# Performance work log

Hardware: AMD Instinct MI355X
Metric: run time of the kernel (lower is better)

The kernel has to match this reference:

```python
import jax, jax.numpy as jnp
import numpy as np
import math

V, D, NL, P, B, L = 32000, 512, 4, 8, 2, 2048

def _ln(x, g, b, eps=1e-5):
    m = x.mean(-1, keepdims=True)
    v = ((x - m) ** 2).mean(-1, keepdims=True)
    return (x - m) / jnp.sqrt(v + eps) * g + b

def setup_inputs() -> dict:
    key = jax.random.key(0)
    ks = jax.random.split(key, 20)
    r = lambda k, shp, s: jax.random.normal(k, shp, dtype=jnp.float32) * s
    return {
        "tokens": jax.random.randint(ks[0], (B, L), 0, V),
        "embed": r(ks[1], (V, D), 0.02),
        "ln_scale": jnp.ones((NL, D), jnp.float32),
        "ln_bias": jnp.zeros((NL, D), jnp.float32),
        "phase_W": r(ks[2], (NL, D, P), 1.0 / math.sqrt(D)),
        "phase_b": jnp.zeros((NL, P), jnp.float32),
        "amp_W": r(ks[3], (NL, D, P), 1.0 / math.sqrt(D)),
        "amp_b": jnp.zeros((NL, P), jnp.float32),
        "value_W": r(ks[4], (NL, D, D), 1.0 / math.sqrt(D)),
        "value_b": jnp.zeros((NL, D), jnp.float32),
        "out_ln_scale": jnp.ones((NL, D), jnp.float32),
        "out_ln_bias": jnp.zeros((NL, D), jnp.float32),
        "out_W": r(ks[5], (NL, D, D), 1.0 / math.sqrt(D)),
        "out_b": jnp.zeros((NL, D), jnp.float32),
        "normout_scale": jnp.ones((D,), jnp.float32),
        "normout_bias": jnp.zeros((D,), jnp.float32),
        "head_W": r(ks[6], (D, V), 1.0 / math.sqrt(D)),
        "head_b": jnp.zeros((V,), jnp.float32),
    }

def _phasor(x, pW, pb, aW, ab, vW, vb, oLNs, oLNb, oW, ob):
    # x: [B,L,D]
    phase = jnp.tanh(x @ pW + pb) * jnp.pi            # [B,L,P]
    amp = jax.nn.softplus(x @ aW + ab) + 0.1          # [B,L,P]
    value = x @ vW + vb                               # [B,L,D]
    # (value[...,None,:] * cos_p[...,:,None] * amp[...,:,None]).sum(-2)
    # == value * sum_p(amp * cos_p)  -- identical math, no [B,L,P,D] intermediate
    coef_r = (amp * jnp.cos(phase)).sum(-1, keepdims=True)
    coef_i = (amp * jnp.sin(phase)).sum(-1, keepdims=True)
    mem_r = jnp.cumsum(value * coef_r, axis=1)
    mem_i = jnp.cumsum(value * coef_i, axis=1)
    retrieved = (mem_r + mem_i) / math.sqrt(x.shape[1])
    return x + (_ln(retrieved, oLNs, oLNb) @ oW + ob)

def reference(tokens, embed, ln_scale, ln_bias, phase_W, phase_b, amp_W, amp_b,
              value_W, value_b, out_ln_scale, out_ln_bias, out_W, out_b,
              normout_scale, normout_bias, head_W, head_b):
    h = embed[tokens]                                 # [B,L,D]
    for i in range(NL):
        hn = _ln(h, ln_scale[i], ln_bias[i])
        h = h + _phasor(hn, phase_W[i], phase_b[i], amp_W[i], amp_b[i],
                        value_W[i], value_b[i], out_ln_scale[i], out_ln_bias[i],
                        out_W[i], out_b[i])
    return _ln(h, normout_scale, normout_bias) @ head_W + head_b  # [B,L,V]
```

## Files before the change

### kernel.cpp

```cpp
#include <hip/hip_runtime.h>
#include <math.h>

#define D 512
#define P 8
#define NL 4
#define BB 2
#define LL 2048
#define VV 32000
#define MTOK (BB*LL)
#define CH 128
#define NCH (LL/CH)

__device__ __forceinline__ float softplusf(float x){
    if (x > 20.f) return x;
    return log1pf(expf(x));
}

__device__ __forceinline__ unsigned short f2bf(float f){
    unsigned int u = __float_as_uint(f);
    unsigned int r = (u + 0x7fffu + ((u >> 16) & 1u)) >> 16;
    return (unsigned short)r;
}
__device__ __forceinline__ float bf2f(unsigned short h){
    return __uint_as_float((unsigned int)h << 16);
}

typedef __attribute__((ext_vector_type(8))) short short8;
typedef __attribute__((ext_vector_type(4))) float f32x4;

__device__ __forceinline__ void gload16(const void* g, void* l){
    __builtin_amdgcn_global_load_lds(
        (const __attribute__((address_space(1))) void*)g,
        (__attribute__((address_space(3))) void*)l, 16, 0, 0);
}

__global__ void gather_kernel(const int* __restrict__ tokens,
                              const float* __restrict__ embed,
                              float* __restrict__ h){
    int t = blockIdx.x;
    int tok = tokens[t];
    const float4* src = (const float4*)(embed + (size_t)tok * D);
    float4* dst = (float4*)(h + (size_t)t * D);
    dst[threadIdx.x] = src[threadIdx.x];
}

__global__ void ln_kernel(const float* __restrict__ x,
                          const float* __restrict__ g,
                          const float* __restrict__ b,
                          float* __restrict__ y){
    int t = blockIdx.x;
    int tid = threadIdx.x;
    const float4* xr = (const float4*)(x + (size_t)t * D);
    float4 v = xr[tid];
    float s = v.x + v.y + v.z + v.w;
    float q = v.x*v.x + v.y*v.y + v.z*v.z + v.w*v.w;
    #pragma unroll
    for (int off = 32; off; off >>= 1){
        s += __shfl_down(s, off);
        q += __shfl_down(q, off);
    }
    __shared__ float red[4];
    int wid = tid >> 6, lane = tid & 63;
    if (lane == 0){ red[wid] = s; red[2 + wid] = q; }
    __syncthreads();
    float mean = (red[0] + red[1]) * (1.f / D);
    float var  = (red[2] + red[3]) * (1.f / D) - mean * mean;
    float rstd = rsqrtf(var + 1e-5f);
    float4 gg = ((const float4*)g)[tid];
    float4 bb = ((const float4*)b)[tid];
    float4 o;
    o.x = (v.x - mean) * rstd * gg.x + bb.x;
    o.y = (v.y - mean) * rstd * gg.y + bb.y;
    o.z = (v.z - mean) * rstd * gg.z + bb.z;
    o.w = (v.w - mean) * rstd * gg.w + bb.w;
    ((float4*)(y + (size_t)t * D))[tid] = o;
}

__global__ void proj_kernel(const float* __restrict__ hn,
                            const float* __restrict__ pW, const float* __restrict__ pb,
                            const float* __restrict__ aW, const float* __restrict__ ab,
                            float* __restrict__ cbuf){
    int wid = threadIdx.x >> 6;
    int lane = threadIdx.x & 63;
    int t = blockIdx.x * 4 + wid;
    const float* x = hn + (size_t)t * D;
    float ph[P] = {0.f,0.f,0.f,0.f,0.f,0.f,0.f,0.f};
    float am[P] = {0.f,0.f,0.f,0.f,0.f,0.f,0.f,0.f};
    int d0 = lane * 8;
    #pragma unroll
    for (int j = 0; j < 8; j++){
        float xv = x[d0 + j];
        const float* pr = pW + (size_t)(d0 + j) * P;
        const float* ar = aW + (size_t)(d0 + j) * P;
        #pragma unroll
        for (int p = 0; p < P; p++){ ph[p] += xv * pr[p]; am[p] += xv * ar[p]; }
    }
    #pragma unroll
    for (int off = 32; off; off >>= 1){
        #pragma unroll
        for (int p = 0; p < P; p++){
            ph[p] += __shfl_down(ph[p], off);
            am[p] += __shfl_down(am[p], off);
        }
    }
    if (lane == 0){
        float c = 0.f;
        #pragma unroll
        for (int p = 0; p < P; p++){
            float phase = tanhf(ph[p] + pb[p]) * 3.14159265358979323846f;
            float amp = softplusf(am[p] + ab[p]) + 0.1f;
            c += amp * (cosf(phase) + sinf(phase));
        }
        cbuf[t] = c;
    }
}

__global__ __launch_bounds__(256) void gemm_kernel(
    const float* __restrict__ A, const float* __restrict__ B,
    const float* __restrict__ bias, const float* __restrict__ rowscale,
    const float* __restrict__ R1, const float* __restrict__ R2,
    float* __restrict__ C, int M, int N, int K)
{
    __shared__ float As[16][64];
    __shared__ float Bs[16][64];
    int bn = blockIdx.x * 64, bm = blockIdx.y * 64;
    int tid = threadIdx.x;
    int tx = tid & 15, ty = tid >> 4;
    float acc[4][4] = {};
    int arow = tid >> 2, acol = (tid & 3) * 4;
    int brow = tid >> 4, bcol = (tid & 15) * 4;
    for (int k0 = 0; k0 < K; k0 += 16){
        float4 av = *(const float4*)(A + (size_t)(bm + arow) * K + k0 + acol);
        As[acol + 0][arow] = av.x; As[acol + 1][arow] = av.y;
        As[acol + 2][arow] = av.z; As[acol + 3][arow] = av.w;
        float4 bv = *(const float4*)(B + (size_t)(k0 + brow) * N + bn + bcol);
        *(float4*)(&Bs[brow][bcol]) = bv;
        __syncthreads();
        #pragma unroll
        for (int k = 0; k < 16; k++){
            float ar[4], br[4];
            #pragma unroll
            for (int i = 0; i < 4; i++) ar[i] = As[k][ty * 4 + i];
            #pragma unroll
            for (int j = 0; j < 4; j++) br[j] = Bs[k][tx * 4 + j];
            #pragma unroll
            for (int i = 0; i < 4; i++)
                #pragma unroll
                for (int j = 0; j < 4; j++)
                    acc[i][j] += ar[i] * br[j];
        }
        __syncthreads();
    }
    float4 bi = *(const float4*)(bias + bn + tx * 4);
    #pragma unroll
    for (int i = 0; i < 4; i++){
        int m = bm + ty * 4 + i;
        float rs = rowscale ? rowscale[m] : 1.f;
        size_t idx = (size_t)m * N + bn + tx * 4;
        float4 v;
        v.x = (acc[i][0] + bi.x) * rs;
        v.y = (acc[i][1] + bi.y) * rs;
        v.z = (acc[i][2] + bi.z) * rs;
        v.w = (acc[i][3] + bi.w) * rs;
        if (R1){
            float4 r = *(const float4*)(R1 + idx);
            v.x += r.x; v.y += r.y; v.z += r.z; v.w += r.w;
        }
        if (R2){
            float4 r = *(const float4*)(R2 + idx);
            v.x += r.x; v.y += r.y; v.z += r.z; v.w += r.w;
        }
        *(float4*)(C + idx) = v;
    }
}

__global__ void scan1_kernel(const float* __restrict__ s, float* __restrict__ partial){
    int id = blockIdx.x;
    int b = id >> 5;
    int rem = id & 31;
    int ch = rem >> 1;
    int d = (rem & 1) * 256 + threadIdx.x;
    const float* base = s + ((size_t)b * LL + (size_t)ch * CH) * D + d;
    float sum = 0.f;
    for (int l = 0; l < CH; l++) sum += base[(size_t)l * D];
    partial[((size_t)b * D + d) * NCH + ch] = sum;
}

__global__ void scan2_kernel(float* __restrict__ partial){
    int t = blockIdx.x * 256 + threadIdx.x;
    float run = 0.f;
    float* p = partial + (size_t)t * NCH;
    for (int ch = 0; ch < NCH; ch++){ float v = p[ch]; p[ch] = run; run += v; }
}

__global__ void scan3_kernel(const float* __restrict__ s, const float* __restrict__ partial,
                             float* __restrict__ ret){
    int id = blockIdx.x;
    int b = id >> 5;
    int rem = id & 31;
    int ch = rem >> 1;
    int d = (rem & 1) * 256 + threadIdx.x;
    float run = partial[((size_t)b * D + d) * NCH + ch];
    const float invs = 0.022097086912079608f;
    const float* base = s + ((size_t)b * LL + (size_t)ch * CH) * D + d;
    float* obase = ret + ((size_t)b * LL + (size_t)ch * CH) * D + d;
    for (int l = 0; l < CH; l++){
        run += base[(size_t)l * D];
        obase[(size_t)l * D] = run * invs;
    }
}


__global__ void convA_kernel(const float* __restrict__ x, unsigned short* __restrict__ A2){
    int t = blockIdx.x, tid = threadIdx.x;
    float4 v = ((const float4*)(x + (size_t)t * D))[tid];
    ushort4 h, l;
    h.x = f2bf(v.x); l.x = f2bf(v.x - bf2f(h.x));
    h.y = f2bf(v.y); l.y = f2bf(v.y - bf2f(h.y));
    h.z = f2bf(v.z); l.z = f2bf(v.z - bf2f(h.z));
    h.w = f2bf(v.w); l.w = f2bf(v.w - bf2f(h.w));
    size_t o = (size_t)t * 1024 + (size_t)tid * 4;
    *(ushort4*)(A2 + o)       = h;
    *(ushort4*)(A2 + o + 512) = l;
}

__global__ __launch_bounds__(256) void convB_kernel(const float* __restrict__ Bsrc,
                                                    unsigned short* __restrict__ Bt){
    __shared__ float tile[64][65];
    int n0 = blockIdx.x * 64;
    int k0 = blockIdx.y * 64;
    int tid = threadIdx.x;
    #pragma unroll
    for (int ph = 0; ph < 4; ph++){
        int idx = ph * 256 + tid;
        int r = idx >> 4;
        int c4 = idx & 15;
        float4 v = *(const float4*)(Bsrc + (size_t)(k0 + r) * VV + n0 + c4 * 4);
        tile[r][c4*4+0] = v.x; tile[r][c4*4+1] = v.y;
        tile[r][c4*4+2] = v.z; tile[r][c4*4+3] = v.w;
    }
    __syncthreads();
    int nn = tid >> 2;
    int kb = tid & 3;
    size_t orow = (size_t)(n0 + nn) * 1024;
    #pragma unroll
    for (int j4 = 0; j4 < 4; j4++){
        int kk = kb * 16 + j4 * 4;
        ushort4 h4, l4;
        float v0 = tile[kk + 0][nn], v1 = tile[kk + 1][nn];
        float v2 = tile[kk + 2][nn], v3 = tile[kk + 3][nn];
        h4.x = f2bf(v0); l4.x = f2bf(v0 - bf2f(h4.x));
        h4.y = f2bf(v1); l4.y = f2bf(v1 - bf2f(h4.y));
        h4.z = f2bf(v2); l4.z = f2bf(v2 - bf2f(h4.z));
        h4.w = f2bf(v3); l4.w = f2bf(v3 - bf2f(h4.w));
        size_t o = orow + (size_t)(k0 + kk);
        *(ushort4*)(Bt + o)       = h4;
        *(ushort4*)(Bt + o + 512) = l4;
    }
}

__global__ __launch_bounds__(256) void head_mfma_kernel(
    const unsigned short* __restrict__ A2,
    const unsigned short* __restrict__ Bt,
    const float* __restrict__ bias,
    float* __restrict__ C)
{
    __shared__ unsigned short As[2][4096];
    __shared__ unsigned short Bs[2][4096];
    const int bm = blockIdx.x * 128;
    const int bn = blockIdx.y * 128;
    const int tid  = threadIdx.x;
    const int lane = tid & 63;
    const int wave = tid >> 6;
    const int wr = wave >> 1, wc = wave & 1;

    const int srow = wave * 32 + (lane >> 2);
    const int scol = (lane & 3) * 8;
    const unsigned short* Ag0 = A2 + (size_t)(bm + srow) * 1024 + scol;
    const unsigned short* Ag1 = Ag0 + (size_t)16 * 1024;
    const unsigned short* Bg0 = Bt + (size_t)(bn + srow) * 1024 + scol;
    const unsigned short* Bg1 = Bg0 + (size_t)16 * 1024;

    f32x4 acc[4][4] = {};

    const int frow = lane & 15;
    const int kq   = lane >> 4;
    const int abase = (wr * 64 + frow) * 32 + kq * 8;
    const int bbase = (wc * 64 + frow) * 32 + kq * 8;

    auto stagef = [&](int buf, int ko){
        int ka = (ko < 512) ? ko : ko - 512;
        int kb = (ko >= 1024) ? ko - 1024 : ko;
        gload16(Ag0 + ka, &As[buf][wave * 1024]);
        gload16(Ag1 + ka, &As[buf][wave * 1024 + 512]);
        gload16(Bg0 + kb, &Bs[buf][wave * 1024]);
        gload16(Bg1 + kb, &Bs[buf][wave * 1024 + 512]);
    };

    stagef(0, 0);
    __syncthreads();

    for (int t = 0; t < 48; ++t){
        int cur = t & 1;
        if (t < 47) stagef(cur ^ 1, (t + 1) * 32);
        const unsigned short* Ab = &As[cur][0];
        const unsigned short* Bb = &Bs[cur][0];
        short8 af[4], bv[4];
        #pragma unroll
        for (int f = 0; f < 4; f++){
            af[f] = *(const short8*)(Ab + abase + f * 512);
            bv[f] = *(const short8*)(Bb + bbase + f * 512);
        }
        #pragma unroll
        for (int i = 0; i < 4; i++)
            #pragma unroll
            for (int j = 0; j < 4; j++)
                acc[i][j] = __builtin_amdgcn_mfma_f32_16x16x32_bf16(af[i], bv[j], acc[i][j], 0, 0, 0);
        __syncthreads();
    }

    #pragma unroll
    for (int j = 0; j < 4; j++){
        int col = bn + wc * 64 + j * 16 + frow;
        float bi = bias[col];
        #pragma unroll
        for (int i = 0; i < 4; i++){
            int row0 = bm + wr * 64 + i * 16 + kq * 4;
            #pragma unroll
            for (int r = 0; r < 4; r++)
                C[(size_t)(row0 + r) * VV + col] = acc[i][j][r] + bi;
        }
    }
}

extern "C" void kernel_launch(void* const* d_in, const int* in_sizes, int n_in,
                              void* d_out, int out_size, void* d_ws, size_t ws_size,
                              hipStream_t stream) {
    const int*   tokens        = (const int*)  d_in[0];
    const float* embed         = (const float*)d_in[1];
    const float* ln_scale      = (const float*)d_in[2];
    const float* ln_bias       = (const float*)d_in[3];
    const float* phase_W       = (const float*)d_in[4];
    const float* phase_b       = (const float*)d_in[5];
    const float* amp_W         = (const float*)d_in[6];
    const float* amp_b         = (const float*)d_in[7];
    const float* value_W       = (const float*)d_in[8];
    const float* value_b       = (const float*)d_in[9];
    const float* out_ln_scale  = (const float*)d_in[10];
    const float* out_ln_bias   = (const float*)d_in[11];
    const float* out_W         = (const float*)d_in[12];
    const float* out_b         = (const float*)d_in[13];
    const float* normout_scale = (const float*)d_in[14];
    const float* normout_bias  = (const float*)d_in[15];
    const float* head_W        = (const float*)d_in[16];
    const float* head_b        = (const float*)d_in[17];
    float* out = (float*)d_out;

    float* ws   = (float*)d_ws;
    float* h    = ws;
    float* hn   = h    + (size_t)MTOK*D;
    float* sbuf = hn   + (size_t)MTOK*D;
    float* rbuf = sbuf + (size_t)MTOK*D;
    float* cbuf = rbuf + (size_t)MTOK*D;
    float* part = cbuf + MTOK;

    size_t used_f = (size_t)4*MTOK*D + MTOK + (size_t)BB*D*NCH;
    size_t abf_f  = (used_f + 255) & ~(size_t)255;
    size_t bbf_f  = abf_f + (size_t)MTOK * 1024 / 2;
    size_t need   = (bbf_f + (size_t)VV * 1024 / 2) * sizeof(float);
    unsigned short* Abf = (unsigned short*)(ws + abf_f);
    unsigned short* Bbf = (unsigned short*)(ws + bbf_f);
    bool fast = (ws_size >= need);

    gather_kernel<<<MTOK, 128, 0, stream>>>(tokens, embed, h);

    for (int i = 0; i < NL; i++){
        ln_kernel<<<MTOK, 128, 0, stream>>>(h, ln_scale + i*D, ln_bias + i*D, hn);
        proj_kernel<<<MTOK/4, 256, 0, stream>>>(hn,
            phase_W + (size_t)i*D*P, phase_b + i*P,
            amp_W   + (size_t)i*D*P, amp_b   + i*P, cbuf);
        dim3 g1(D/64, MTOK/64);
        gemm_kernel<<<g1, 256, 0, stream>>>(hn, value_W + (size_t)i*D*D, value_b + i*D,
                                            cbuf, nullptr, nullptr, sbuf, MTOK, D, D);
        scan1_kernel<<<64, 256, 0, stream>>>(sbuf, part);
        scan2_kernel<<<4, 256, 0, stream>>>(part);
        scan3_kernel<<<64, 256, 0, stream>>>(sbuf, part, rbuf);
        ln_kernel<<<MTOK, 128, 0, stream>>>(rbuf, out_ln_scale + i*D, out_ln_bias + i*D, rbuf);
        gemm_kernel<<<g1, 256, 0, stream>>>(rbuf, out_W + (size_t)i*D*D, out_b + i*D,
                                            nullptr, h, hn, h, MTOK, D, D);
    }

    ln_kernel<<<MTOK, 128, 0, stream>>>(h, normout_scale, normout_bias, hn);

    if (fast){
        convA_kernel<<<MTOK, 128, 0, stream>>>(hn, Abf);
        convB_kernel<<<dim3(VV/64, D/64), 256, 0, stream>>>(head_W, Bbf);
        head_mfma_kernel<<<dim3(MTOK/128, VV/128), 256, 0, stream>>>(Abf, Bbf, head_b, out);
    } else {
        dim3 gh(VV/64, MTOK/64);
        gemm_kernel<<<gh, 256, 0, stream>>>(hn, head_W, head_b,
                                            nullptr, nullptr, nullptr, out, MTOK, VV, D);
    }
}
```

Baseline: 1.669 ms.

## Switch matmuls to fp16 split-A MFMA and move layer GEMMs to tensor cores

Replaces the bf16 hi/lo split on both operands with fp16, splitting only the activations into hi+lo while keeping weights as a single fp16 copy. This cuts the head GEMM K loop from 48 to 32 steps and halves the weight buffer. It also adds a gemm16 MFMA kernel plus a convW pre-conversion, so the per-layer value and output GEMMs run on matrix cores instead of the fp32 gemm_kernel. The scan chunk size drops from 128 to 32 for more parallelism. Rounding the weights to fp16 alone reduces accuracy, and the extra convA passes per layer add memory traffic.

```diff
diff --git a/kernel.cpp b/kernel.cpp
--- a/kernel.cpp
+++ b/kernel.cpp
@@ -8,7 +8,7 @@
 #define LL 2048
 #define VV 32000
 #define MTOK (BB*LL)
-#define CH 128
+#define CH 32
 #define NCH (LL/CH)
 
 __device__ __forceinline__ float softplusf(float x){
@@ -16,16 +16,16 @@
     return log1pf(expf(x));
 }
 
-__device__ __forceinline__ unsigned short f2bf(float f){
-    unsigned int u = __float_as_uint(f);
-    unsigned int r = (u + 0x7fffu + ((u >> 16) & 1u)) >> 16;
-    return (unsigned short)r;
-}
-__device__ __forceinline__ float bf2f(unsigned short h){
-    return __uint_as_float((unsigned int)h << 16);
-}
-
-typedef __attribute__((ext_vector_type(8))) short short8;
+__device__ __forceinline__ unsigned short f2h_u(float f){
+    _Float16 h = (_Float16)f;
+    union { _Float16 h; unsigned short u; } cv; cv.h = h; return cv.u;
+}
+__device__ __forceinline__ float h_lo_residual(float f, unsigned short hu){
+    union { unsigned short u; _Float16 h; } cv; cv.u = hu;
+    return f - (float)cv.h;
+}
+
+typedef __attribute__((ext_vector_type(8))) _Float16 f16x8;
 typedef __attribute__((ext_vector_type(4))) float f32x4;
 
 __device__ __forceinline__ void gload16(const void* g, void* l){
@@ -176,8 +176,8 @@
 
 __global__ void scan1_kernel(const float* __restrict__ s, float* __restrict__ partial){
     int id = blockIdx.x;
-    int b = id >> 5;
-    int rem = id & 31;
+    int b = id >> 7;
+    int rem = id & 127;
     int ch = rem >> 1;
     int d = (rem & 1) * 256 + threadIdx.x;
     const float* base = s + ((size_t)b * LL + (size_t)ch * CH) * D + d;
@@ -196,8 +196,8 @@
 __global__ void scan3_kernel(const float* __restrict__ s, const float* __restrict__ partial,
                              float* __restrict__ ret){
     int id = blockIdx.x;
-    int b = id >> 5;
-    int rem = id & 31;
+    int b = id >> 7;
+    int rem = id & 127;
     int ch = rem >> 1;
     int d = (rem & 1) * 256 + threadIdx.x;
     float run = partial[((size_t)b * D + d) * NCH + ch];
@@ -215,10 +215,10 @@
     int t = blockIdx.x, tid = threadIdx.x;
     float4 v = ((const float4*)(x + (size_t)t * D))[tid];
     ushort4 h, l;
-    h.x = f2bf(v.x); l.x = f2bf(v.x - bf2f(h.x));
-    h.y = f2bf(v.y); l.y = f2bf(v.y - bf2f(h.y));
-    h.z = f2bf(v.z); l.z = f2bf(v.z - bf2f(h.z));
-    h.w = f2bf(v.w); l.w = f2bf(v.w - bf2f(h.w));
+    h.x = f2h_u(v.x); l.x = f2h_u(h_lo_residual(v.x, h.x));
+    h.y = f2h_u(v.y); l.y = f2h_u(h_lo_residual(v.y, h.y));
+    h.z = f2h_u(v.z); l.z = f2h_u(h_lo_residual(v.z, h.z));
+    h.w = f2h_u(v.w); l.w = f2h_u(h_lo_residual(v.w, h.w));
     size_t o = (size_t)t * 1024 + (size_t)tid * 4;
     *(ushort4*)(A2 + o)       = h;
     *(ushort4*)(A2 + o + 512) = l;
@@ -242,20 +242,51 @@
     __syncthreads();
     int nn = tid >> 2;
     int kb = tid & 3;
-    size_t orow = (size_t)(n0 + nn) * 1024;
+    size_t orow = (size_t)(n0 + nn) * 512;
     #pragma unroll
     for (int j4 = 0; j4 < 4; j4++){
         int kk = kb * 16 + j4 * 4;
-        ushort4 h4, l4;
-        float v0 = tile[kk + 0][nn], v1 = tile[kk + 1][nn];
-        float v2 = tile[kk + 2][nn], v3 = tile[kk + 3][nn];
-        h4.x = f2bf(v0); l4.x = f2bf(v0 - bf2f(h4.x));
-        h4.y = f2bf(v1); l4.y = f2bf(v1 - bf2f(h4.y));
-        h4.z = f2bf(v2); l4.z = f2bf(v2 - bf2f(h4.z));
-        h4.w = f2bf(v3); l4.w = f2bf(v3 - bf2f(h4.w));
-        size_t o = orow + (size_t)(k0 + kk);
-        *(ushort4*)(Bt + o)       = h4;
-        *(ushort4*)(Bt + o + 512) = l4;
+        ushort4 h4;
+        h4.x = f2h_u(tile[kk + 0][nn]);
+        h4.y = f2h_u(tile[kk + 1][nn]);
+        h4.z = f2h_u(tile[kk + 2][nn]);
+        h4.w = f2h_u(tile[kk + 3][nn]);
+        *(ushort4*)(Bt + orow + (size_t)(k0 + kk)) = h4;
+    }
+}
+
+__global__ __launch_bounds__(256) void convW_kernel(const float* __restrict__ vW,
+                                                    const float* __restrict__ oW,
+                                                    unsigned short* __restrict__ Wt){
+    __shared__ float tile[64][65];
+    int m = blockIdx.z;
+    const float* src = (m < NL) ? (vW + (size_t)m * D * D) : (oW + (size_t)(m - NL) * D * D);
+    unsigned short* dst = Wt + (size_t)m * D * D;
+    int n0 = blockIdx.x * 64;
+    int k0 = blockIdx.y * 64;
+    int tid = threadIdx.x;
+    #pragma unroll
+    for (int ph = 0; ph < 4; ph++){
+        int idx = ph * 256 + tid;
+        int r = idx >> 4;
+        int c4 = idx & 15;
+        float4 v = *(const float4*)(src + (size_t)(k0 + r) * D + n0 + c4 * 4);
+        tile[r][c4*4+0] = v.x; tile[r][c4*4+1] = v.y;
+        tile[r][c4*4+2] = v.z; tile[r][c4*4+3] = v.w;
+    }
+    __syncthreads();
+    int nn = tid >> 2;
+    int kb = tid & 3;
+    size_t orow = (size_t)(n0 + nn) * 512;
+    #pragma unroll
+    for (int j4 = 0; j4 < 4; j4++){
+        int kk = kb * 16 + j4 * 4;
+        ushort4 h4;
+        h4.x = f2h_u(tile[kk + 0][nn]);
+        h4.y = f2h_u(tile[kk + 1][nn]);
+        h4.z = f2h_u(tile[kk + 2][nn]);
+        h4.w = f2h_u(tile[kk + 3][nn]);
+        *(ushort4*)(dst + orow + (size_t)(k0 + kk)) = h4;
     }
 }
 
@@ -278,8 +309,8 @@
     const int scol = (lane & 3) * 8;
     const unsigned short* Ag0 = A2 + (size_t)(bm + srow) * 1024 + scol;
     const unsigned short* Ag1 = Ag0 + (size_t)16 * 1024;
-    const unsigned short* Bg0 = Bt + (size_t)(bn + srow) * 1024 + scol;
-    const unsigned short* Bg1 = Bg0 + (size_t)16 * 1024;
+    const unsigned short* Bg0 = Bt + (size_t)(bn + srow) * 512 + scol;
+    const unsigned short* Bg1 = Bg0 + (size_t)16 * 512;
 
     f32x4 acc[4][4] = {};
 
@@ -289,10 +320,9 @@
     const int bbase = (wc * 64 + frow) * 32 + kq * 8;
 
     auto stagef = [&](int buf, int ko){
-        int ka = (ko < 512) ? ko : ko - 512;
-        int kb = (ko >= 1024) ? ko - 1024 : ko;
-        gload16(Ag0 + ka, &As[buf][wave * 1024]);
-        gload16(Ag1 + ka, &As[buf][wave * 1024 + 512]);
+        int kb = ko & 511;
+        gload16(Ag0 + ko, &As[buf][wave * 1024]);
+        gload16(Ag1 + ko, &As[buf][wave * 1024 + 512]);
         gload16(Bg0 + kb, &Bs[buf][wave * 1024]);
         gload16(Bg1 + kb, &Bs[buf][wave * 1024 + 512]);
     };
@@ -300,22 +330,22 @@
     stagef(0, 0);
     __syncthreads();
 
-    for (int t = 0; t < 48; ++t){
+    for (int t = 0; t < 32; ++t){
         int cur = t & 1;
-        if (t < 47) stagef(cur ^ 1, (t + 1) * 32);
+        if (t < 31) stagef(cur ^ 1, (t + 1) * 32);
         const unsigned short* Ab = &As[cur][0];
         const unsigned short* Bb = &Bs[cur][0];
-        short8 af[4], bv[4];
+        f16x8 af[4], bv[4];
         #pragma unroll
         for (int f = 0; f < 4; f++){
-            af[f] = *(const short8*)(Ab + abase + f * 512);
-            bv[f] = *(const short8*)(Bb + bbase + f * 512);
+            af[f] = *(const f16x8*)(const void*)(Ab + abase + f * 512);
+            bv[f] = *(const f16x8*)(const void*)(Bb + bbase + f * 512);
         }
         #pragma unroll
         for (int i = 0; i < 4; i++)
             #pragma unroll
             for (int j = 0; j < 4; j++)
-                acc[i][j] = __builtin_amdgcn_mfma_f32_16x16x32_bf16(af[i], bv[j], acc[i][j], 0, 0, 0);
+                acc[i][j] = __builtin_amdgcn_mfma_f32_16x16x32_f16(af[i], bv[j], acc[i][j], 0, 0, 0);
         __syncthreads();
     }
 
@@ -329,6 +359,86 @@
             #pragma unroll
             for (int r = 0; r < 4; r++)
                 C[(size_t)(row0 + r) * VV + col] = acc[i][j][r] + bi;
+        }
+    }
+}
+
+__global__ __launch_bounds__(256) void gemm16_kernel(
+    const unsigned short* __restrict__ A2,
+    const unsigned short* __restrict__ Bt,
+    const float* __restrict__ bias,
+    const float* __restrict__ rowscale,
+    const float* __restrict__ R1, const float* __restrict__ R2,
+    float* __restrict__ C)
+{
+    __shared__ unsigned short As[2][4096];
+    __shared__ unsigned short Bs[2][2048];
+    const int bm = blockIdx.x * 128;
+    const int bn = blockIdx.y * 64;
+    const int tid  = threadIdx.x;
+    const int lane = tid & 63;
+    const int wave = tid >> 6;
+    const int wr = wave >> 1, wc = wave & 1;
+
+    const int srow = wave * 32 + (lane >> 2);
+    const int srb  = wave * 16 + (lane >> 2);
+    const int scol = (lane & 3) * 8;
+    const unsigned short* Ag0 = A2 + (size_t)(bm + srow) * 1024 + scol;
+    const unsigned short* Ag1 = Ag0 + (size_t)16 * 1024;
+    const unsigned short* Bg  = Bt + (size_t)(bn + srb) * 512 + scol;
+
+    f32x4 acc[4][2] = {};
+
+    const int frow = lane & 15;
+    const int kq   = lane >> 4;
+    const int abase = (wr * 64 + frow) * 32 + kq * 8;
+    const int bbase = (wc * 32 + frow) * 32 + kq * 8;
+
+    auto stagef = [&](int buf, int ko){
+        int kb = ko & 511;
+        gload16(Ag0 + ko, &As[buf][wave * 1024]);
+        gload16(Ag1 + ko, &As[buf][wave * 1024 + 512]);
+        gload16(Bg + kb,  &Bs[buf][wave * 512]);
+    };
+
+    stagef(0, 0);
+    __syncthreads();
+
+    for (int t = 0; t < 32; ++t){
+        int cur = t & 1;
+        if (t < 31) stagef(cur ^ 1, (t + 1) * 32);
+        const unsigned short* Ab = &As[cur][0];
+        const unsigned short* Bb = &Bs[cur][0];
+        f16x8 af[4], bv[2];
+        #pragma unroll
+        for (int f = 0; f < 4; f++) af[f] = *(const f16x8*)(const void*)(Ab + abase + f * 512);
+        #pragma unroll
+        for (int f = 0; f < 2; f++) bv[f] = *(const f16x8*)(const void*)(Bb + bbase + f * 512);
+        #pragma unroll
+        for (int i = 0; i < 4; i++)
+            #pragma unroll
+            for (int j = 0; j < 2; j++)
+                acc[i][j] = __builtin_amdgcn_mfma_f32_16x16x32_f16(af[i], bv[j], acc[i][j], 0, 0, 0);
+        __syncthreads();
+    }
+
+    #pragma unroll
+    for (int j = 0; j < 2; j++){
+        int col = bn + wc * 32 + j * 16 + frow;
+        float bi = bias[col];
+        #pragma unroll
+        for (int i = 0; i < 4; i++){
+            int row0 = bm + wr * 64 + i * 16 + kq * 4;
+            #pragma unroll
+            for (int r = 0; r < 4; r++){
+                int row = row0 + r;
+                size_t idx = (size_t)row * D + col;
+                float v = acc[i][j][r] + bi;
+                if (rowscale) v *= rowscale[row];
+                if (R1) v += R1[idx];
+                if (R2) v += R2[idx];
+                C[idx] = v;
+            }
         }
     }
 }
@@ -366,35 +476,53 @@
 
     size_t used_f = (size_t)4*MTOK*D + MTOK + (size_t)BB*D*NCH;
     size_t abf_f  = (used_f + 255) & ~(size_t)255;
-    size_t bbf_f  = abf_f + (size_t)MTOK * 1024 / 2;
-    size_t need   = (bbf_f + (size_t)VV * 1024 / 2) * sizeof(float);
+    size_t bbf_f  = abf_f + (size_t)MTOK * 512;
+    size_t wt_f   = bbf_f + (size_t)VV * 256;
+    size_t need   = (wt_f + (size_t)2*NL*D*D/2) * sizeof(float);
     unsigned short* Abf = (unsigned short*)(ws + abf_f);
     unsigned short* Bbf = (unsigned short*)(ws + bbf_f);
+    unsigned short* Wt  = (unsigned short*)(ws + wt_f);
     bool fast = (ws_size >= need);
 
     gather_kernel<<<MTOK, 128, 0, stream>>>(tokens, embed, h);
+    if (fast){
+        convW_kernel<<<dim3(D/64, D/64, 2*NL), 256, 0, stream>>>(value_W, out_W, Wt);
+        convB_kernel<<<dim3(VV/64, D/64), 256, 0, stream>>>(head_W, Bbf);
+    }
 
     for (int i = 0; i < NL; i++){
         ln_kernel<<<MTOK, 128, 0, stream>>>(h, ln_scale + i*D, ln_bias + i*D, hn);
         proj_kernel<<<MTOK/4, 256, 0, stream>>>(hn,
             phase_W + (size_t)i*D*P, phase_b + i*P,
             amp_W   + (size_t)i*D*P, amp_b   + i*P, cbuf);
-        dim3 g1(D/64, MTOK/64);
-        gemm_kernel<<<g1, 256, 0, stream>>>(hn, value_W + (size_t)i*D*D, value_b + i*D,
-                                            cbuf, nullptr, nullptr, sbuf, MTOK, D, D);
-        scan1_kernel<<<64, 256, 0, stream>>>(sbuf, part);
+        if (fast){
+            convA_kernel<<<MTOK, 128, 0, stream>>>(hn, Abf);
+            gemm16_kernel<<<dim3(MTOK/128, D/64), 256, 0, stream>>>(Abf,
+                Wt + (size_t)i*D*D, value_b + i*D, cbuf, nullptr, nullptr, sbuf);
+        } else {
+            dim3 g1(D/64, MTOK/64);
+            gemm_kernel<<<g1, 256, 0, stream>>>(hn, value_W + (size_t)i*D*D, value_b + i*D,
+                                                cbuf, nullptr, nullptr, sbuf, MTOK, D, D);
+        }
+        scan1_kernel<<<256, 256, 0, stream>>>(sbuf, part);
         scan2_kernel<<<4, 256, 0, stream>>>(part);
-        scan3_kernel<<<64, 256, 0, stream>>>(sbuf, part, rbuf);
+        scan3_kernel<<<256, 256, 0, stream>>>(sbuf, part, rbuf);
         ln_kernel<<<MTOK, 128, 0, stream>>>(rbuf, out_ln_scale + i*D, out_ln_bias + i*D, rbuf);
-        gemm_kernel<<<g1, 256, 0, stream>>>(rbuf, out_W + (size_t)i*D*D, out_b + i*D,
-                                            nullptr, h, hn, h, MTOK, D, D);
+        if (fast){
+            convA_kernel<<<MTOK, 128, 0, stream>>>(rbuf, Abf);
+            gemm16_kernel<<<dim3(MTOK/128, D/64), 256, 0, stream>>>(Abf,
+                Wt + (size_t)(NL + i)*D*D, out_b + i*D, nullptr, h, hn, h);
+        } else {
+            dim3 g1(D/64, MTOK/64);
+            gemm_kernel<<<g1, 256, 0, stream>>>(rbuf, out_W + (size_t)i*D*D, out_b + i*D,
+                                                nullptr, h, hn, h, MTOK, D, D);
+        }
     }
 
     ln_kernel<<<MTOK, 128, 0, stream>>>(h, normout_scale, normout_bias, hn);
 
     if (fast){
         convA_kernel<<<MTOK, 128, 0, stream>>>(hn, Abf);
-        convB_kernel<<<dim3(VV/64, D/64), 256, 0, stream>>>(head_W, Bbf);
         head_mfma_kernel<<<dim3(MTOK/128, VV/128), 256, 0, stream>>>(Abf, Bbf, head_b, out);
     } else {
         dim3 gh(VV/64, MTOK/64);
```

Result: faster. 1.445 ms (-13.4%).
